# Kernel optimization log

Hardware: AMD Instinct MI355X
Metric: run time of the kernel (lower is better)

## Reference

```python
import jax, jax.numpy as jnp
import numpy as np

N = 100000        # nodes
E = 1600000       # edges (avg degree 16)
HID = 64          # hidden_dim
IN = 64           # input_dim
H = 4             # GAT heads
C = HID // H      # per-head channels (hidden//4)
LN_EPS = 1e-5
NEG_SLOPE = 0.2   # PyG GATConv default


def setup_inputs() -> dict:
    key = jax.random.key(0)
    ks = jax.random.split(key, 12)

    def nrm(k, shape, fan_in):
        return jax.random.normal(k, shape, jnp.float32) / np.sqrt(fan_in).astype(np.float32)

    x = jax.random.normal(ks[0], (N, IN), jnp.float32)
    edge_index = jax.random.randint(ks[1], (2, E), 0, N, jnp.int32)
    return {
        "x": x,
        "edge_index": edge_index,
        "emb_W": nrm(ks[2], (HID, IN), IN),
        "emb_b": jnp.zeros((HID,), jnp.float32),
        "e8_W": nrm(ks[3], (3, HID, HID), HID),
        "gat_W": nrm(ks[4], (3, HID, H * C), HID),
        "att_src": nrm(ks[5], (3, H, C), C),
        "att_dst": nrm(ks[6], (3, H, C), C),
        "gat_b": jnp.zeros((3, HID), jnp.float32),
        "fus_W": nrm(ks[7], (3, HID, 2 * HID), 2 * HID),
        "fus_b": jnp.zeros((3, HID), jnp.float32),
        "ln_g": jnp.ones((3, HID), jnp.float32),
        "ln_b": jnp.zeros((3, HID), jnp.float32),
        "r_W1": nrm(ks[8], (HID // 2, HID), HID),
        "r_b1": jnp.zeros((HID // 2,), jnp.float32),
        "r_W2": nrm(ks[9], (1, HID // 2), HID // 2),
        "r_b2": jnp.zeros((1,), jnp.float32),
    }


def _forward(x, edge_index, emb_W, emb_b, e8_W, gat_W, att_src, att_dst, gat_b,
             fus_W, fus_b, ln_g, ln_b, r_W1, r_b1, r_W2, r_b2):
    n = x.shape[0]
    row, col = edge_index[0], edge_index[1]

    # --- E8 symmetric normalization (depends only on graph; constant across layers) ---
    deg = jax.ops.segment_sum(jnp.ones_like(col, dtype=jnp.float32), col, num_segments=n)
    dinv = jnp.where(deg > 0, deg ** -0.5, 0.0)           # inf -> 0 as in torch code
    vals = dinv[row] * dinv[col]                           # [E]

    # --- GAT self-loops (PyG GATConv add_self_loops=True) ---
    loop = jnp.arange(n, dtype=row.dtype)
    src = jnp.concatenate([row, loop])                     # [E+N]
    dst = jnp.concatenate([col, loop])                     # [E+N]

    h = x @ emb_W.T + emb_b                                # embedding: [N, HID]

    for i in range(3):  # fixed 3 structurally-distinct blocks
        res = h
        # E8: sparse adj matmul then linear (no bias)
        x_e8 = jax.ops.segment_sum(vals[:, None] * h[col], row, num_segments=n) @ e8_W[i].T

        # GATConv (heads=4, concat)
        g = (h @ gat_W[i]).reshape(n, H, C)                # [N,H,C]
        a_s = (g * att_src[i]).sum(-1)                     # [N,H]
        a_d = (g * att_dst[i]).sum(-1)                     # [N,H]
        e = jax.nn.leaky_relu(a_s[src] + a_d[dst], NEG_SLOPE)   # [E+N,H]
        m = jax.lax.stop_gradient(jax.ops.segment_max(e, dst, num_segments=n))
        ee = jnp.exp(e - m[dst])
        s = jax.ops.segment_sum(ee, dst, num_segments=n)   # [N,H], >0 (self-loops)
        alpha = ee / s[dst]                                # per-dst softmax
        x_gat = jax.ops.segment_sum(alpha[:, :, None] * g[src], dst, num_segments=n)
        x_gat = x_gat.reshape(n, H * C) + gat_b[i]

        # fusion + residual + LayerNorm + ReLU (dropout is identity in eval)
        h = jnp.concatenate([x_e8, x_gat], axis=-1) @ fus_W[i].T + fus_b[i]
        h = h + res
        mu = h.mean(-1, keepdims=True)
        var = ((h - mu) ** 2).mean(-1, keepdims=True)
        h = (h - mu) * jax.lax.rsqrt(var + LN_EPS) * ln_g[i] + ln_b[i]
        h = jax.nn.relu(h)

    h1 = jax.nn.relu(h @ r_W1.T + r_b1)                    # [N, HID//2]
    return jax.nn.sigmoid(h1 @ r_W2.T + r_b2)              # [N, 1]


def reference(x, edge_index, emb_W, emb_b, e8_W, gat_W, att_src, att_dst, gat_b,
              fus_W, fus_b, ln_g, ln_b, r_W1, r_b1, r_W2, r_b2):
    return _forward(x, edge_index, emb_W, emb_b, e8_W, gat_W, att_src, att_dst, gat_b,
                    fus_W, fus_b, ln_g, ln_b, r_W1, r_b1, r_W2, r_b2)
```

## Files before the change

### kernel.cpp

```cpp
#include <hip/hip_runtime.h>
#include <hip/hip_bf16.h>
#include <hip/hip_fp16.h>

typedef __hip_bfloat16 bf16;
typedef unsigned short ushort_t;
typedef unsigned short us8 __attribute__((ext_vector_type(8)));
typedef _Float16 half8 __attribute__((ext_vector_type(8)));
typedef float f32x4 __attribute__((ext_vector_type(4)));

#define NEG 0.2f
#define LNEPS 1e-5f
#define BWD 512

__device__ __forceinline__ int plaus(unsigned int lo){
    lo &= 0x7FFFu;
    if (lo == 0) return 1;
    unsigned int ex = (lo >> 7) & 0xFF;
    return (ex >= 100 && ex <= 140) ? 1 : 0;
}

__device__ __forceinline__ float decode_slot(const ushort_t* s, long long i, int fl){
    long long base = i << fl;
    unsigned int hi = s[base + fl];
    unsigned int lo = s[base];
    unsigned int bits = (hi << 16) | (lo * (unsigned int)fl);
    return __uint_as_float(bits);
}

__device__ __forceinline__ unsigned encf(float f){
    int b = __float_as_int(f);
    return (b >= 0) ? ((unsigned)b | 0x80000000u) : (unsigned)(~b);
}
__device__ __forceinline__ float decf(unsigned k){
    return (k & 0x80000000u) ? __uint_as_float(k & 0x7FFFFFFFu)
                             : __uint_as_float(~k);
}

#define P_TOTAL 56577
#define CONV_BLKS 222
__global__ __launch_bounds__(256) void k_init(const void* p0, const void* p1, const void* p2,
        const void* p3, const void* p4, const void* p5, const void* p6, const void* p7,
        const void* p8, const void* p9, const void* p10, const void* p11, const void* p12,
        const void* p13, const void* p14, const void* xs,
        const int* __restrict__ row, const int* __restrict__ col, int E, int NBK,
        int* flags, float* P, int* bcnt, unsigned* mxsu){
    __shared__ int lh[512];
    int t = threadIdx.x;
    if (blockIdx.x >= CONV_BLKS){
        int hb = blockIdx.x - CONV_BLKS;
        for (int i = t; i < 2*NBK; i += 256) lh[i] = 0;
        __syncthreads();
        for (long long e = (long long)hb*256 + t; e < E; e += (long long)256*256){
            atomicAdd(&lh[row[e] >> 9], 1);
            atomicAdd(&lh[NBK + (col[e] >> 9)], 1);
        }
        __syncthreads();
        for (int i = t; i < 2*NBK; i += 256){
            int v = lh[i];
            if (v) atomicAdd(&bcnt[i], v);
        }
        return;
    }
    if (blockIdx.x == 0){
        if (t < 9){
            const void* dt[9] = {xs, p0, p2, p3, p4, p5, p7, p11, p13};
            const ushort_t* w = (const ushort_t*)dt[t];
            int all_bf = 1;
            for (int i = 0; i < 16; i++) all_bf &= plaus((unsigned int)w[i]);
            flags[t] = all_bf ? 0 : 1;
        } else if (t == 9){
            const ushort_t* w = (const ushort_t*)p9;
            flags[9] = (w[0] == 0x3F80u) ? 0 : 1;
        }
        if (t < 32) mxsu[t] = 0u;
    }
    int idx = blockIdx.x*256 + t;
    if (idx >= P_TOTAL) return;
    const int sizes[15] = {4096,64,12288,12288,192,192,192,24576,192,192,192,2048,32,32,1};
    const int fidx[15]  = {1,  -1,  2,    3,    4,  5,  -1, 6,    -1, 9,  -1, 7,   -1,8, -1};
    const void* ptrs[15] = {p0,p1,p2,p3,p4,p5,p6,p7,p8,p9,p10,p11,p12,p13,p14};
    int s = 0, base = 0;
    while (idx - base >= sizes[s]){ base += sizes[s]; s++; }
    int li = idx - base;
    int fi = fidx[s];
    int fl = 0;
    if (fi == 9){
        const ushort_t* w = (const ushort_t*)ptrs[s];
        fl = (w[0] == 0x3F80u) ? 0 : 1;
    } else if (fi >= 0){
        const ushort_t* w = (const ushort_t*)ptrs[s];
        int all_bf = 1;
        for (int i = 0; i < 16; i++) all_bf &= plaus((unsigned int)w[i]);
        fl = all_bf ? 0 : 1;
    }
    P[idx] = decode_slot((const ushort_t*)ptrs[s], li, fl);
}

#define PRW_B0 (3*8192)
#define PRW_B1 (PRW_B0 + 192)
#define PRW_B2 (PRW_B1 + 3*5120)
__global__ __launch_bounds__(256) void kb_scanprew(const int* __restrict__ bcnt,
        int* __restrict__ bptr_r, int* __restrict__ bptr_c,
        int* __restrict__ bcur_r, int* __restrict__ bcur_c, int NBK, int E,
        const float* __restrict__ fus_W, const float* __restrict__ e8_W,
        const float* __restrict__ gat_b, const float* __restrict__ fus_b,
        const float* __restrict__ gat_W, const float* __restrict__ att_src,
        const float* __restrict__ att_dst,
        _Float16* __restrict__ Bfrag, float* __restrict__ b2c, _Float16* __restrict__ Bg){
    __shared__ int sh[256];
    int t = threadIdx.x;
    if (blockIdx.x < 2){
        int side = blockIdx.x;
        const int* c = bcnt + side*NBK;
        int* bp = side ? bptr_c : bptr_r;
        int* bc = side ? bcur_c : bcur_r;
        int v = (t < NBK) ? c[t] : 0;
        sh[t] = v; __syncthreads();
        for (int off = 1; off < 256; off <<= 1){
            int add = (t >= off) ? sh[t-off] : 0;
            __syncthreads();
            sh[t] += add;
            __syncthreads();
        }
        if (t < NBK){ int e = sh[t] - v; bp[t] = e; bc[t] = e; }
        if (t == 0) bp[NBK] = E;
        return;
    }
    int idx = (blockIdx.x - 2)*256 + t;
    if (idx < PRW_B0){
        int i = idx / 8192; int rem = idx & 8191;
        int j = rem & 7, lane = (rem >> 3) & 63, kk = (rem >> 9) & 3, tt = rem >> 11;
        int k = kk*32 + (lane >> 4)*8 + j;
        int n = tt*16 + (lane & 15);
        float v;
        if (k < 64){
            const float* fw = fus_W + (size_t)i*8192 + (size_t)n*128;
            const float* ew = e8_W + (size_t)i*4096;
            float acc = 0.f;
            for (int p = 0; p < 64; p++) acc += fw[p] * ew[p*64 + k];
            v = acc;
        } else {
            v = fus_W[(size_t)i*8192 + (size_t)n*128 + 64 + (k - 64)];
        }
        Bfrag[idx] = (_Float16)v;
    } else if (idx < PRW_B1){
        int t2 = idx - PRW_B0;
        int i = t2 >> 6, j = t2 & 63;
        const float* fw = fus_W + (size_t)i*8192 + (size_t)j*128 + 64;
        float acc = fus_b[i*64+j];
        for (int p = 0; p < 64; p++) acc += gat_b[i*64+p] * fw[p];
        b2c[t2] = acc;
    } else if (idx < PRW_B2){
        int t3 = idx - PRW_B1;
        int i = t3 / 5120; int rem = t3 % 5120;
        int j = rem & 7, lane = (rem >> 3) & 63, kk = (rem >> 9) & 1, tt = rem >> 10;
        int k = kk*32 + (lane >> 4)*8 + j;
        int nn = lane & 15;
        float v;
        if (tt < 4){
            v = gat_W[(size_t)i*4096 + k*64 + (tt*16 + nn)];
        } else if (nn < 8){
            int hx = nn >> 1;
            const float* att = (nn & 1) ? att_dst : att_src;
            float acc = 0.f;
            for (int cc = 0; cc < 16; cc++)
                acc += gat_W[(size_t)i*4096 + k*64 + hx*16 + cc] * att[i*64 + hx*16 + cc];
            v = acc;
        } else {
            v = 0.f;
        }
        Bg[t3] = (_Float16)v;
    }
}

__global__ __launch_bounds__(1024) void kb_bin(const int* __restrict__ row,
        const int* __restrict__ col, int* __restrict__ bcur_r, int* __restrict__ bcur_c,
        uint2* __restrict__ stage_r, uint2* __restrict__ stage_c, int NBK, int E){
    __shared__ int lh[256], lbase[256];
    int side = blockIdx.x >> 8;
    int bid  = blockIdx.x & 255;
    const int* key = side ? col : row;
    const int* pay = side ? row : col;
    int* bcur = side ? bcur_c : bcur_r;
    uint2* stage = side ? stage_c : stage_r;
    int t = threadIdx.x;
    for (long long tile = (long long)bid*1024; tile < E; tile += (long long)256*1024){
        for (int i = t; i < NBK; i += 1024) lh[i] = 0;
        __syncthreads();
        int e = (int)tile + t;
        int k = 0, p = 0, b = -1, rank = 0;
        if (e < E){
            k = key[e]; p = pay[e]; b = k >> 9;
            rank = atomicAdd(&lh[b], 1);
        }
        __syncthreads();
        for (int i = t; i < NBK; i += 1024){
            int c = lh[i];
            lbase[i] = c ? atomicAdd(&bcur[i], c) : 0;
        }
        __syncthreads();
        if (b >= 0) stage[lbase[b] + rank] = make_uint2((unsigned)k, (unsigned)p);
        __syncthreads();
    }
}

__global__ __launch_bounds__(1024) void kb_place(const uint2* __restrict__ stage_r,
        const uint2* __restrict__ stage_c, const int* __restrict__ bptr_r,
        const int* __restrict__ bptr_c, int* __restrict__ ptr_r, int* __restrict__ ptr_c,
        int* __restrict__ re_col, int* __restrict__ ce_row,
        float* __restrict__ dinv, int NBK, int N, int E){
    __shared__ int lcnt[BWD], lsc[BWD], lcur[BWD];
    int side = blockIdx.x >= NBK;
    int b = blockIdx.x - (side ? NBK : 0);
    const uint2* stage = side ? stage_c : stage_r;
    const int* bptr = side ? bptr_c : bptr_r;
    int* ptr = side ? ptr_c : ptr_r;
    int* outarr = side ? ce_row : re_col;
    int wantdinv = side;
    int s = bptr[b], e = bptr[b+1];
    int nbase = b << 9;
    int t = threadIdx.x;
    if (t < BWD) lcnt[t] = 0;
    __syncthreads();
    for (int i = s + t; i < e; i += 1024)
        atomicAdd(&lcnt[stage[i].x - nbase], 1);
    __syncthreads();
    if (t < BWD) lsc[t] = lcnt[t];
    __syncthreads();
    for (int off = 1; off < BWD; off <<= 1){
        int add = (t >= off && t < BWD) ? lsc[t-off] : 0;
        __syncthreads();
        if (t < BWD) lsc[t] += add;
        __syncthreads();
    }
    if (t < BWD){
        int node = nbase + t;
        int excl = lsc[t] - lcnt[t];
        lcur[t] = excl;
        if (node < N){
            ptr[node] = s + excl;
            if (wantdinv) dinv[node] = lcnt[t] > 0 ? rsqrtf((float)lcnt[t]) : 0.f;
        }
    }
    if (b == 0 && t == 0) ptr[N] = E;
    __syncthreads();
    for (int i = s + t; i < e; i += 1024){
        uint2 rec = stage[i];
        int pos = s + atomicAdd(&lcur[rec.x - nbase], 1);
        outarr[pos] = (int)rec.y;
    }
}

__global__ __launch_bounds__(256) void k_embed_g(const ushort_t* __restrict__ xs,
        const int* __restrict__ flags, const float* __restrict__ W,
        const float* __restrict__ b, const float* __restrict__ dinv,
        const _Float16* __restrict__ Bgn,
        __half* __restrict__ h16, __half* __restrict__ ht16, __half* __restrict__ G16,
        float* __restrict__ a_s, float* __restrict__ a_d, float* __restrict__ mxs, int N){
    __shared__ float redm[4][8];
    __shared__ _Float16 tbuf[4][1024];
    int lane = threadIdx.x & 63;
    int wv = threadIdx.x >> 6;
    int q = lane >> 4, c = lane & 15;
    _Float16* tb = tbuf[wv];
    int fl = flags[0];
    half8 Be[4][2];
    #pragma unroll
    for (int t = 0; t < 4; t++){
        #pragma unroll
        for (int kk = 0; kk < 2; kk++){
            half8 v;
            #pragma unroll
            for (int j = 0; j < 8; j++)
                v[j] = (_Float16)W[(t*16 + c)*64 + kk*32 + q*8 + j];
            Be[t][kk] = v;
        }
    }
    half8 Bg[5][2];
    const half8* Bgp = (const half8*)Bgn;
    #pragma unroll
    for (int t = 0; t < 5; t++)
        #pragma unroll
        for (int kk = 0; kk < 2; kk++)
            Bg[t][kk] = Bgp[(t*2+kk)*64 + lane];
    float bj[4];
    #pragma unroll
    for (int t = 0; t < 4; t++) bj[t] = b[t*16 + c];
    float lmax = -1e30f;
    int tiles = (N + 15) >> 4;
    int wid = (blockIdx.x*blockDim.x + threadIdx.x) >> 6;
    int nw  = (gridDim.x*blockDim.x) >> 6;
    for (int tile = wid; tile < tiles; tile += nw){
        int nb = tile << 4;
        int anode = nb + c; if (anode >= N) anode = N - 1;
        half8 A0, A1;
        #pragma unroll
        for (int j = 0; j < 8; j++){
            A0[j] = (_Float16)decode_slot(xs, (long long)anode*64 + q*8 + j, fl);
            A1[j] = (_Float16)decode_slot(xs, (long long)anode*64 + 32 + q*8 + j, fl);
        }
        f32x4 acc[4];
        #pragma unroll
        for (int t = 0; t < 4; t++){
            f32x4 z = {0.f, 0.f, 0.f, 0.f};
            z = __builtin_amdgcn_mfma_f32_16x16x32_f16(A0, Be[t][0], z, 0, 0, 0);
            z = __builtin_amdgcn_mfma_f32_16x16x32_f16(A1, Be[t][1], z, 0, 0, 0);
            acc[t] = z;
        }
        #pragma unroll
        for (int r = 0; r < 4; r++){
            int node = nb + q*4 + r;
            int nd2 = q*4 + r;
            #pragma unroll
            for (int t = 0; t < 4; t++){
                float out = acc[t][r] + bj[t];
                int byte = nd2*128 + (t*16 + c)*2;
                byte ^= (nd2 & 7) << 4;
                *(_Float16*)((char*)tb + byte) = (_Float16)out;
                if (node < N){
                    h16[(size_t)node*64 + t*16 + c] = __float2half(out);
                    ht16[(size_t)node*64 + t*16 + c] = __float2half(dinv[node]*out);
                }
            }
        }
        int b0 = (c*128 + 16*q) ^ ((c & 7) << 4);
        int b1 = (c*128 + 64 + 16*q) ^ ((c & 7) << 4);
        half8 A0g = *(half8*)((char*)tb + b0);
        half8 A1g = *(half8*)((char*)tb + b1);
        f32x4 gacc[5];
        #pragma unroll
        for (int t = 0; t < 5; t++){
            f32x4 z = {0.f, 0.f, 0.f, 0.f};
            z = __builtin_amdgcn_mfma_f32_16x16x32_f16(A0g, Bg[t][0], z, 0, 0, 0);
            z = __builtin_amdgcn_mfma_f32_16x16x32_f16(A1g, Bg[t][1], z, 0, 0, 0);
            gacc[t] = z;
        }
        #pragma unroll
        for (int r = 0; r < 4; r++) lmax = fmaxf(lmax, gacc[4][r]);
        #pragma unroll
        for (int r = 0; r < 4; r++){
            int node = nb + q*4 + r;
            if (node < N){
                #pragma unroll
                for (int t = 0; t < 4; t++)
                    G16[(size_t)node*64 + t*16 + c] = __float2half(gacc[t][r]);
                if (c < 8){
                    int hx = c >> 1;
                    if (c & 1) a_d[node*4+hx] = gacc[4][r];
                    else       a_s[node*4+hx] = gacc[4][r];
                }
            }
        }
    }
    lmax = fmaxf(lmax, __shfl_xor(lmax, 16));
    lmax = fmaxf(lmax, __shfl_xor(lmax, 32));
    if (lane < 8) redm[wv][lane] = lmax;
    __syncthreads();
    if (threadIdx.x < 8){
        float m = fmaxf(fmaxf(redm[0][threadIdx.x], redm[1][threadIdx.x]),
                        fmaxf(redm[2][threadIdx.x], redm[3][threadIdx.x]));
        int hx = threadIdx.x >> 1;
        int ix = (threadIdx.x & 1) ? 4 + hx : hx;
        atomicMax((unsigned*)mxs + ix, encf(m));
    }
}

__device__ __forceinline__ float leaky(float t){ return t > 0.f ? t : NEG*t; }

__global__ __launch_bounds__(256) void k_gather(const __half* __restrict__ ht16,
        const __half* __restrict__ G16,
        const float* __restrict__ a_s, const float* __restrict__ a_d,
        const float* __restrict__ mxs, const float* __restrict__ dinv,
        const int* __restrict__ row_ptr, const int* __restrict__ re_col,
        const int* __restrict__ col_ptr, const int* __restrict__ ce_row,
        __half* __restrict__ Aj16, __half* __restrict__ xg16, int N){
    int lane = threadIdx.x & 63;
    int grp  = lane >> 3;
    int sub  = lane & 7;
    int hh   = sub >> 1;
    int wid  = (blockIdx.x*blockDim.x + threadIdx.x) >> 6;
    int v    = wid*8 + grp;
    if (v >= N) return;
    const us8* htb = (const us8*)ht16;
    const us8* gb  = (const us8*)G16;
    const unsigned* mu = (const unsigned*)mxs;
    float sh = leaky(decf(mu[hh]) + decf(mu[4+hh]));
    int rs = row_ptr[v], re = row_ptr[v+1];
    float a0[8] = {0,0,0,0,0,0,0,0}, a1[8] = {0,0,0,0,0,0,0,0};
    float a2[8] = {0,0,0,0,0,0,0,0}, a3[8] = {0,0,0,0,0,0,0,0};
    int i = rs;
    for (; i + 3 < re; i += 4){
        us8 q0 = htb[(size_t)re_col[i]*8 + sub];
        us8 q1 = htb[(size_t)re_col[i+1]*8 + sub];
        us8 q2 = htb[(size_t)re_col[i+2]*8 + sub];
        us8 q3 = htb[(size_t)re_col[i+3]*8 + sub];
        #pragma unroll
        for (int j = 0; j < 8; j++){
            a0[j] += __half2float(__ushort_as_half(q0[j]));
            a1[j] += __half2float(__ushort_as_half(q1[j]));
            a2[j] += __half2float(__ushort_as_half(q2[j]));
            a3[j] += __half2float(__ushort_as_half(q3[j]));
        }
    }
    for (; i < re; i++){
        us8 q0 = htb[(size_t)re_col[i]*8 + sub];
        #pragma unroll
        for (int j = 0; j < 8; j++) a0[j] += __half2float(__ushort_as_half(q0[j]));
    }
    float dv = dinv[v];
    us8 pa;
    #pragma unroll
    for (int j = 0; j < 8; j++)
        pa[j] = __half_as_ushort(__float2half(dv*((a0[j]+a1[j]) + (a2[j]+a3[j]))));
    ((us8*)Aj16)[(size_t)v*8 + sub] = pa;
    float adv = a_d[v*4+hh];
    float eesl = __expf(leaky(a_s[v*4+hh] + adv) - sh);
    float s0 = eesl, s1 = 0.f, s2 = 0.f, s3 = 0.f;
    {
        us8 g0 = gb[(size_t)v*8 + sub];
        #pragma unroll
        for (int j = 0; j < 8; j++){
            a0[j] = eesl * __half2float(__ushort_as_half(g0[j]));
            a1[j] = 0.f; a2[j] = 0.f; a3[j] = 0.f;
        }
    }
    int cs = col_ptr[v], ce = col_ptr[v+1];
    i = cs;
    for (; i + 3 < ce; i += 4){
        int r0 = ce_row[i], r1 = ce_row[i+1], r2 = ce_row[i+2], r3 = ce_row[i+3];
        float e0 = __expf(leaky(a_s[r0*4+hh] + adv) - sh);
        float e1 = __expf(leaky(a_s[r1*4+hh] + adv) - sh);
        float e2 = __expf(leaky(a_s[r2*4+hh] + adv) - sh);
        float e3 = __expf(leaky(a_s[r3*4+hh] + adv) - sh);
        us8 q0 = gb[(size_t)r0*8 + sub];
        us8 q1 = gb[(size_t)r1*8 + sub];
        us8 q2 = gb[(size_t)r2*8 + sub];
        us8 q3 = gb[(size_t)r3*8 + sub];
        #pragma unroll
        for (int j = 0; j < 8; j++){
            a0[j] += e0 * __half2float(__ushort_as_half(q0[j]));
            a1[j] += e1 * __half2float(__ushort_as_half(q1[j]));
            a2[j] += e2 * __half2float(__ushort_as_half(q2[j]));
            a3[j] += e3 * __half2float(__ushort_as_half(q3[j]));
        }
        s0 += e0; s1 += e1; s2 += e2; s3 += e3;
    }
    for (; i < ce; i++){
        int r0 = ce_row[i];
        float e0 = __expf(leaky(a_s[r0*4+hh] + adv) - sh);
        us8 q0 = gb[(size_t)r0*8 + sub];
        #pragma unroll
        for (int j = 0; j < 8; j++) a0[j] += e0 * __half2float(__ushort_as_half(q0[j]));
        s0 += e0;
    }
    float inv = 1.f/((s0+s1)+(s2+s3));
    us8 px;
    #pragma unroll
    for (int j = 0; j < 8; j++)
        px[j] = __half_as_ushort(__float2half(((a0[j]+a1[j]) + (a2[j]+a3[j]))*inv));
    ((us8*)xg16)[(size_t)v*8 + sub] = px;
}

__global__ __launch_bounds__(256) void k_fuse_g(
        const __half* __restrict__ Aj16, const __half* __restrict__ xg16,
        const float* __restrict__ dinv, __half* __restrict__ h16,
        __half* __restrict__ ht16,
        const _Float16* __restrict__ Bfrag, const float* __restrict__ b2c,
        const float* __restrict__ ln_g, const float* __restrict__ ln_b,
        const _Float16* __restrict__ Bgn, __half* __restrict__ G16,
        float* __restrict__ a_s, float* __restrict__ a_d,
        float* __restrict__ mxs_next, int N){
    __shared__ float redm[4][8];
    __shared__ _Float16 tbuf[4][1024];
    int lane = threadIdx.x & 63;
    int wv = threadIdx.x >> 6;
    int q = lane >> 4, c = lane & 15;
    _Float16* tb = tbuf[wv];
    half8 B[4][4];
    const half8* Bp = (const half8*)Bfrag;
    #pragma unroll
    for (int t = 0; t < 4; t++)
        #pragma unroll
        for (int kk = 0; kk < 4; kk++)
            B[t][kk] = Bp[(t*4+kk)*64 + lane];
    half8 Bg[5][2];
    const half8* Bgp = (const half8*)Bgn;
    #pragma unroll
    for (int t = 0; t < 5; t++)
        #pragma unroll
        for (int kk = 0; kk < 2; kk++)
            Bg[t][kk] = Bgp[(t*2+kk)*64 + lane];
    float bj[4], lg[4], lb[4];
    #pragma unroll
    for (int t = 0; t < 4; t++){
        int n = t*16 + c;
        bj[t] = b2c[n]; lg[t] = ln_g[n]; lb[t] = ln_b[n];
    }
    float lmax = -1e30f;
    int tiles = (N + 15) >> 4;
    int wid = (blockIdx.x*blockDim.x + threadIdx.x) >> 6;
    int nw  = (gridDim.x*blockDim.x) >> 6;
    for (int tile = wid; tile < tiles; tile += nw){
        int nb = tile << 4;
        int anode = nb + c; if (anode >= N) anode = N - 1;
        const half8* ap = (const half8*)(Aj16 + (size_t)anode*64);
        const half8* xp = (const half8*)(xg16 + (size_t)anode*64);
        half8 A0 = ap[q];
        half8 A1 = ap[4 + q];
        half8 A2 = xp[q];
        half8 A3 = xp[4 + q];
        f32x4 acc[4];
        #pragma unroll
        for (int t = 0; t < 4; t++){
            f32x4 z = {0.f, 0.f, 0.f, 0.f};
            z = __builtin_amdgcn_mfma_f32_16x16x32_f16(A0, B[t][0], z, 0, 0, 0);
            z = __builtin_amdgcn_mfma_f32_16x16x32_f16(A1, B[t][1], z, 0, 0, 0);
            z = __builtin_amdgcn_mfma_f32_16x16x32_f16(A2, B[t][2], z, 0, 0, 0);
            z = __builtin_amdgcn_mfma_f32_16x16x32_f16(A3, B[t][3], z, 0, 0, 0);
            acc[t] = z;
        }
        float y[4][4];
        #pragma unroll
        for (int r = 0; r < 4; r++){
            int node = nb + q*4 + r;
            int nd = node < N ? node : N - 1;
            #pragma unroll
            for (int t = 0; t < 4; t++)
                y[t][r] = acc[t][r] + bj[t]
                        + __half2float(h16[(size_t)nd*64 + t*16 + c]);
        }
        #pragma unroll
        for (int r = 0; r < 4; r++){
            int node = nb + q*4 + r;
            float s = (y[0][r] + y[1][r]) + (y[2][r] + y[3][r]);
            #pragma unroll
            for (int o = 1; o < 16; o <<= 1) s += __shfl_xor(s, o);
            float mu = s * (1.f/64.f);
            float d0 = y[0][r]-mu, d1 = y[1][r]-mu, d2 = y[2][r]-mu, d3 = y[3][r]-mu;
            float var = (d0*d0 + d1*d1) + (d2*d2 + d3*d3);
            #pragma unroll
            for (int o = 1; o < 16; o <<= 1) var += __shfl_xor(var, o);
            var *= (1.f/64.f);
            float rstd = rsqrtf(var + LNEPS);
            int nd2 = q*4 + r;
            #pragma unroll
            for (int t = 0; t < 4; t++){
                float out = (y[t][r]-mu)*rstd*lg[t] + lb[t];
                out = out > 0.f ? out : 0.f;
                int byte = nd2*128 + (t*16 + c)*2;
                byte ^= (nd2 & 7) << 4;
                *(_Float16*)((char*)tb + byte) = (_Float16)out;
                if (node < N){
                    h16[(size_t)node*64 + t*16 + c] = __float2half(out);
                    ht16[(size_t)node*64 + t*16 + c] = __float2half(dinv[node]*out);
                }
            }
        }
        int b0 = (c*128 + 16*q) ^ ((c & 7) << 4);
        int b1 = (c*128 + 64 + 16*q) ^ ((c & 7) << 4);
        half8 A0g = *(half8*)((char*)tb + b0);
        half8 A1g = *(half8*)((char*)tb + b1);
        f32x4 gacc[5];
        #pragma unroll
        for (int t = 0; t < 5; t++){
            f32x4 z = {0.f, 0.f, 0.f, 0.f};
            z = __builtin_amdgcn_mfma_f32_16x16x32_f16(A0g, Bg[t][0], z, 0, 0, 0);
            z = __builtin_amdgcn_mfma_f32_16x16x32_f16(A1g, Bg[t][1], z, 0, 0, 0);
            gacc[t] = z;
        }
        #pragma unroll
        for (int r = 0; r < 4; r++) lmax = fmaxf(lmax, gacc[4][r]);
        #pragma unroll
        for (int r = 0; r < 4; r++){
            int node = nb + q*4 + r;
            if (node < N){
                #pragma unroll
                for (int t = 0; t < 4; t++)
                    G16[(size_t)node*64 + t*16 + c] = __float2half(gacc[t][r]);
                if (c < 8){
                    int hx = c >> 1;
                    if (c & 1) a_d[node*4+hx] = gacc[4][r];
                    else       a_s[node*4+hx] = gacc[4][r];
                }
            }
        }
    }
    lmax = fmaxf(lmax, __shfl_xor(lmax, 16));
    lmax = fmaxf(lmax, __shfl_xor(lmax, 32));
    if (lane < 8) redm[wv][lane] = lmax;
    __syncthreads();
    if (threadIdx.x < 8){
        float m = fmaxf(fmaxf(redm[0][threadIdx.x], redm[1][threadIdx.x]),
                        fmaxf(redm[2][threadIdx.x], redm[3][threadIdx.x]));
        int hx = threadIdx.x >> 1;
        int ix = (threadIdx.x & 1) ? 4 + hx : hx;
        atomicMax((unsigned*)mxs_next + ix, encf(m));
    }
}

__global__ __launch_bounds__(256) void k_fuse_ro(
        const __half* __restrict__ Aj16, const __half* __restrict__ xg16,
        const __half* __restrict__ h16,
        const _Float16* __restrict__ Bfrag, const float* __restrict__ b2c,
        const float* __restrict__ ln_g, const float* __restrict__ ln_b,
        const float* __restrict__ rW1, const float* __restrict__ rb1,
        const float* __restrict__ rW2, const float* __restrict__ rb2,
        float* __restrict__ out, int N){
    __shared__ _Float16 tbuf[4][1024];
    int lane = threadIdx.x & 63;
    int wv = threadIdx.x >> 6;
    int q = lane >> 4, c = lane & 15;
    _Float16* tb = tbuf[wv];
    half8 B[4][4];
    const half8* Bp = (const half8*)Bfrag;
    #pragma unroll
    for (int t = 0; t < 4; t++)
        #pragma unroll
        for (int kk = 0; kk < 4; kk++)
            B[t][kk] = Bp[(t*4+kk)*64 + lane];
    half8 B1r[2][2];
    #pragma unroll
    for (int t = 0; t < 2; t++){
        #pragma unroll
        for (int kk = 0; kk < 2; kk++){
            half8 v;
            #pragma unroll
            for (int j = 0; j < 8; j++)
                v[j] = (_Float16)rW1[(t*16 + c)*64 + kk*32 + q*8 + j];
            B1r[t][kk] = v;
        }
    }
    float bj[4], lg[4], lb[4];
    #pragma unroll
    for (int t = 0; t < 4; t++){
        int n = t*16 + c;
        bj[t] = b2c[n]; lg[t] = ln_g[n]; lb[t] = ln_b[n];
    }
    float b1v[2] = {rb1[c], rb1[16 + c]};
    float w2a = rW2[c], w2b = rW2[16 + c];
    float b2v = rb2[0];
    int tiles = (N + 15) >> 4;
    int wid = (blockIdx.x*blockDim.x + threadIdx.x) >> 6;
    int nw  = (gridDim.x*blockDim.x) >> 6;
    for (int tile = wid; tile < tiles; tile += nw){
        int nb = tile << 4;
        int anode = nb + c; if (anode >= N) anode = N - 1;
        const half8* ap = (const half8*)(Aj16 + (size_t)anode*64);
        const half8* xp = (const half8*)(xg16 + (size_t)anode*64);
        half8 A0 = ap[q];
        half8 A1 = ap[4 + q];
        half8 A2 = xp[q];
        half8 A3 = xp[4 + q];
        f32x4 acc[4];
        #pragma unroll
        for (int t = 0; t < 4; t++){
            f32x4 z = {0.f, 0.f, 0.f, 0.f};
            z = __builtin_amdgcn_mfma_f32_16x16x32_f16(A0, B[t][0], z, 0, 0, 0);
            z = __builtin_amdgcn_mfma_f32_16x16x32_f16(A1, B[t][1], z, 0, 0, 0);
            z = __builtin_amdgcn_mfma_f32_16x16x32_f16(A2, B[t][2], z, 0, 0, 0);
            z = __builtin_amdgcn_mfma_f32_16x16x32_f16(A3, B[t][3], z, 0, 0, 0);
            acc[t] = z;
        }
        float y[4][4];
        #pragma unroll
        for (int r = 0; r < 4; r++){
            int node = nb + q*4 + r;
            int nd = node < N ? node : N - 1;
            #pragma unroll
            for (int t = 0; t < 4; t++)
                y[t][r] = acc[t][r] + bj[t]
                        + __half2float(h16[(size_t)nd*64 + t*16 + c]);
        }
        #pragma unroll
        for (int r = 0; r < 4; r++){
            float s = (y[0][r] + y[1][r]) + (y[2][r] + y[3][r]);
            #pragma unroll
            for (int o = 1; o < 16; o <<= 1) s += __shfl_xor(s, o);
            float mu = s * (1.f/64.f);
            float d0 = y[0][r]-mu, d1 = y[1][r]-mu, d2 = y[2][r]-mu, d3 = y[3][r]-mu;
            float var = (d0*d0 + d1*d1) + (d2*d2 + d3*d3);
            #pragma unroll
            for (int o = 1; o < 16; o <<= 1) var += __shfl_xor(var, o);
            var *= (1.f/64.f);
            float rstd = rsqrtf(var + LNEPS);
            int nd2 = q*4 + r;
            #pragma unroll
            for (int t = 0; t < 4; t++){
                float outv = (y[t][r]-mu)*rstd*lg[t] + lb[t];
                outv = outv > 0.f ? outv : 0.f;
                int byte = nd2*128 + (t*16 + c)*2;
                byte ^= (nd2 & 7) << 4;
                *(_Float16*)((char*)tb + byte) = (_Float16)outv;
            }
        }
        int b0 = (c*128 + 16*q) ^ ((c & 7) << 4);
        int b1 = (c*128 + 64 + 16*q) ^ ((c & 7) << 4);
        half8 A0g = *(half8*)((char*)tb + b0);
        half8 A1g = *(half8*)((char*)tb + b1);
        f32x4 racc[2];
        #pragma unroll
        for (int t = 0; t < 2; t++){
            f32x4 z = {0.f, 0.f, 0.f, 0.f};
            z = __builtin_amdgcn_mfma_f32_16x16x32_f16(A0g, B1r[t][0], z, 0, 0, 0);
            z = __builtin_amdgcn_mfma_f32_16x16x32_f16(A1g, B1r[t][1], z, 0, 0, 0);
            racc[t] = z;
        }
        #pragma unroll
        for (int r = 0; r < 4; r++){
            int node = nb + q*4 + r;
            float h1a = racc[0][r] + b1v[0]; h1a = h1a > 0.f ? h1a : 0.f;
            float h1b = racc[1][r] + b1v[1]; h1b = h1b > 0.f ? h1b : 0.f;
            float p = h1a*w2a + h1b*w2b;
            p += __shfl_xor(p, 1);
            p += __shfl_xor(p, 2);
            p += __shfl_xor(p, 4);
            p += __shfl_xor(p, 8);
            if (c == 0 && node < N){
                float z = p + b2v;
                out[node] = 1.f/(1.f + __expf(-z));
            }
        }
    }
}

extern "C" void kernel_launch(void* const* d_in, const int* in_sizes, int n_in,
                              void* d_out, int out_size, void* d_ws, size_t ws_size,
                              hipStream_t stream){
    const ushort_t* xs = (const ushort_t*)d_in[0];
    const int*      ei = (const int*)d_in[1];

    int N = in_sizes[0] / 64;
    int E = in_sizes[1] / 2;
    const int* row = ei;
    const int* col = ei + E;
    int NBK = (N + BWD - 1) / BWD;

    size_t stageF = (size_t)2*E;
    size_t mirF   = (size_t)N*32;
    size_t aliasF = stageF > mirF ? stageF : mirF;

    float* f = (float*)d_ws;
    size_t o = 0;
    int*   flags = (int*)(f + o); o += 16;
    float* P     = f + o; o += P_TOTAL + 63;
    __half* h16  = (__half*)(f + o); o += mirF;
    __half* ht16 = (__half*)(f + o); o += mirF;
    __half* G16  = (__half*)(f + o); o += mirF;
    __half* Aj16 = (__half*)(f + o); size_t aoff = o; o += aliasF;
    __half* xg16 = (__half*)(f + o); size_t xoff = o; o += aliasF;
    uint2* stage_r = (uint2*)(f + aoff);
    uint2* stage_c = (uint2*)(f + xoff);
    float* a_s   = f + o; o += (size_t)N*4;
    float* a_d   = f + o; o += (size_t)N*4;
    float* mxs   = f + o; o += 32;
    float* dinv  = f + o; o += ((size_t)N + 15) & ~15ull;
    int* bcnt    = (int*)(f + o); o += 512;
    int* bptr_r  = (int*)(f + o); o += 512;
    int* bptr_c  = (int*)(f + o); o += 512;
    int* bcur_r  = (int*)(f + o); o += 512;
    int* bcur_c  = (int*)(f + o); o += 512;
    int* ptr_r   = (int*)(f + o); o += ((size_t)N + 16) & ~15ull;
    int* ptr_c   = (int*)(f + o); o += ((size_t)N + 16) & ~15ull;
    int* re_col  = (int*)(f + o); o += (size_t)E;
    int* ce_row  = (int*)(f + o); o += (size_t)E;
    float* b2c   = f + o; o += 3*64;
    _Float16* Bfrag = (_Float16*)(f + o); o += 3*4096;
    _Float16* Bg    = (_Float16*)(f + o); o += 3*2560;

    const float* emb_W   = P + 0;
    const float* emb_b   = P + 4096;
    const float* e8_W    = P + 4160;
    const float* gat_W   = P + 16448;
    const float* att_src = P + 28736;
    const float* att_dst = P + 28928;
    const float* gat_b   = P + 29120;
    const float* fus_W   = P + 29312;
    const float* fus_b   = P + 53888;
    const float* ln_g    = P + 54080;
    const float* ln_b    = P + 54272;
    const float* r_W1    = P + 54464;
    const float* r_b1    = P + 56512;
    const float* r_W2    = P + 56544;
    const float* r_b2    = P + 56576;

    hipMemsetAsync(bcnt, 0, 512*sizeof(int), stream);
    k_init<<<CONV_BLKS + 256, 256, 0, stream>>>(
        d_in[2],d_in[3],d_in[4],d_in[5],d_in[6],d_in[7],d_in[8],d_in[9],
        d_in[10],d_in[11],d_in[12],d_in[13],d_in[14],d_in[15],d_in[16],
        d_in[0], row, col, E, NBK, flags, P, bcnt, (unsigned*)mxs);

    int prwblk = (PRW_B2 + 255) / 256;
    kb_scanprew<<<2 + prwblk, 256, 0, stream>>>(bcnt, bptr_r, bptr_c, bcur_r, bcur_c,
                                                NBK, E, fus_W, e8_W, gat_b, fus_b,
                                                gat_W, att_src, att_dst, Bfrag, b2c, Bg);
    kb_bin<<<512, 1024, 0, stream>>>(row, col, bcur_r, bcur_c, stage_r, stage_c, NBK, E);
    kb_place<<<2*NBK, 1024, 0, stream>>>(stage_r, stage_c, bptr_r, bptr_c,
                                         ptr_r, ptr_c, re_col, ce_row, dinv, NBK, N, E);

    int tiles = (N + 15) / 16;
    int fgrid = (tiles + 7) / 8;
    int ggrid = (N + 31) / 32;
    k_embed_g<<<fgrid, 256, 0, stream>>>(xs, flags, emb_W, emb_b, dinv, Bg,
                                         h16, ht16, G16, a_s, a_d, mxs, N);
    for (int i = 0; i < 3; i++){
        k_gather<<<ggrid, 256, 0, stream>>>(ht16, G16, a_s, a_d, mxs + i*8, dinv,
                                            ptr_r, re_col, ptr_c, ce_row,
                                            Aj16, xg16, N);
        if (i < 2){
            k_fuse_g<<<fgrid, 256, 0, stream>>>(Aj16, xg16, dinv, h16, ht16,
                                                Bfrag + (size_t)i*8192, b2c + i*64,
                                                ln_g + i*64, ln_b + i*64,
                                                Bg + (size_t)(i+1)*5120, G16,
                                                a_s, a_d, mxs + (i+1)*8, N);
        } else {
            k_fuse_ro<<<fgrid, 256, 0, stream>>>(Aj16, xg16, h16,
                                                 Bfrag + (size_t)i*8192, b2c + i*64,
                                                 ln_g + i*64, ln_b + i*64,
                                                 r_W1, r_b1, r_W2, r_b2,
                                                 (float*)d_out, N);
        }
    }
}
```

Before: 651.6 us.

## Fuse gather with fusion/LayerNorm epilogue and split GAT projection kernel

The per-node gather of E8 and GAT aggregates is merged with the fusion matmul, residual, LayerNorm and ReLU, and the readout, using scalar FMAs over weights held in LDS. This removes the Aj16/xg16 intermediate round-trips through global memory. The next layer's GAT projection moves into a separate MFMA kernel, k_gat_g, and h/ht are ping-ponged between two buffers. The change also packs staging records into 32 bits and vectorises input loads in the embedding, at the cost of replacing MFMA with per-lane scalar FMA for the 128x64 fusion matmul and adding an LDS-heavy inner loop.

```diff
diff --git a/kernel.cpp b/kernel.cpp
--- a/kernel.cpp
+++ b/kernel.cpp
@@ -6,6 +6,7 @@
 typedef unsigned short ushort_t;
 typedef unsigned short us8 __attribute__((ext_vector_type(8)));
 typedef _Float16 half8 __attribute__((ext_vector_type(8)));
+typedef _Float16 half4v __attribute__((ext_vector_type(4)));
 typedef float f32x4 __attribute__((ext_vector_type(4)));
 
 #define NEG 0.2f
@@ -99,14 +100,16 @@
 #define PRW_B0 (3*8192)
 #define PRW_B1 (PRW_B0 + 192)
 #define PRW_B2 (PRW_B1 + 3*5120)
+#define PRW_B3 (PRW_B2 + 2048)
 __global__ __launch_bounds__(256) void kb_scanprew(const int* __restrict__ bcnt,
         int* __restrict__ bptr_r, int* __restrict__ bptr_c,
         int* __restrict__ bcur_r, int* __restrict__ bcur_c, int NBK, int E,
         const float* __restrict__ fus_W, const float* __restrict__ e8_W,
         const float* __restrict__ gat_b, const float* __restrict__ fus_b,
         const float* __restrict__ gat_W, const float* __restrict__ att_src,
-        const float* __restrict__ att_dst,
-        _Float16* __restrict__ Bfrag, float* __restrict__ b2c, _Float16* __restrict__ Bg){
+        const float* __restrict__ att_dst, const float* __restrict__ r_W1,
+        _Float16* __restrict__ Wt16, float* __restrict__ b2c,
+        _Float16* __restrict__ Bg, _Float16* __restrict__ Wr16){
     __shared__ int sh[256];
     int t = threadIdx.x;
     if (blockIdx.x < 2){
@@ -129,20 +132,18 @@
     int idx = (blockIdx.x - 2)*256 + t;
     if (idx < PRW_B0){
         int i = idx / 8192; int rem = idx & 8191;
-        int j = rem & 7, lane = (rem >> 3) & 63, kk = (rem >> 9) & 3, tt = rem >> 11;
-        int k = kk*32 + (lane >> 4)*8 + j;
-        int n = tt*16 + (lane & 15);
+        int p = rem >> 6, j = rem & 63;
         float v;
-        if (k < 64){
-            const float* fw = fus_W + (size_t)i*8192 + (size_t)n*128;
+        if (p < 64){
+            const float* fw = fus_W + (size_t)i*8192 + (size_t)j*128;
             const float* ew = e8_W + (size_t)i*4096;
             float acc = 0.f;
-            for (int p = 0; p < 64; p++) acc += fw[p] * ew[p*64 + k];
+            for (int q = 0; q < 64; q++) acc += fw[q] * ew[q*64 + p];
             v = acc;
         } else {
-            v = fus_W[(size_t)i*8192 + (size_t)n*128 + 64 + (k - 64)];
-        }
-        Bfrag[idx] = (_Float16)v;
+            v = fus_W[(size_t)i*8192 + (size_t)j*128 + p];
+        }
+        Wt16[idx] = (_Float16)v;
     } else if (idx < PRW_B1){
         int t2 = idx - PRW_B0;
         int i = t2 >> 6, j = t2 & 63;
@@ -170,19 +171,23 @@
             v = 0.f;
         }
         Bg[t3] = (_Float16)v;
+    } else if (idx < PRW_B3){
+        int t4 = idx - PRW_B2;
+        int k = t4 >> 5, j = t4 & 31;
+        Wr16[t4] = (_Float16)r_W1[j*64 + k];
     }
 }
 
 __global__ __launch_bounds__(1024) void kb_bin(const int* __restrict__ row,
         const int* __restrict__ col, int* __restrict__ bcur_r, int* __restrict__ bcur_c,
-        uint2* __restrict__ stage_r, uint2* __restrict__ stage_c, int NBK, int E){
+        unsigned* __restrict__ stage_r, unsigned* __restrict__ stage_c, int NBK, int E){
     __shared__ int lh[256], lbase[256];
     int side = blockIdx.x >> 8;
     int bid  = blockIdx.x & 255;
     const int* key = side ? col : row;
     const int* pay = side ? row : col;
     int* bcur = side ? bcur_c : bcur_r;
-    uint2* stage = side ? stage_c : stage_r;
+    unsigned* stage = side ? stage_c : stage_r;
     int t = threadIdx.x;
     for (long long tile = (long long)bid*1024; tile < E; tile += (long long)256*1024){
         for (int i = t; i < NBK; i += 1024) lh[i] = 0;
@@ -199,31 +204,30 @@
             lbase[i] = c ? atomicAdd(&bcur[i], c) : 0;
         }
         __syncthreads();
-        if (b >= 0) stage[lbase[b] + rank] = make_uint2((unsigned)k, (unsigned)p);
+        if (b >= 0) stage[lbase[b] + rank] = ((unsigned)(k & 511) << 23) | (unsigned)p;
         __syncthreads();
     }
 }
 
-__global__ __launch_bounds__(1024) void kb_place(const uint2* __restrict__ stage_r,
-        const uint2* __restrict__ stage_c, const int* __restrict__ bptr_r,
+__global__ __launch_bounds__(1024) void kb_place(const unsigned* __restrict__ stage_r,
+        const unsigned* __restrict__ stage_c, const int* __restrict__ bptr_r,
         const int* __restrict__ bptr_c, int* __restrict__ ptr_r, int* __restrict__ ptr_c,
         int* __restrict__ re_col, int* __restrict__ ce_row,
         float* __restrict__ dinv, int NBK, int N, int E){
     __shared__ int lcnt[BWD], lsc[BWD], lcur[BWD];
     int side = blockIdx.x >= NBK;
     int b = blockIdx.x - (side ? NBK : 0);
-    const uint2* stage = side ? stage_c : stage_r;
+    const unsigned* stage = side ? stage_c : stage_r;
     const int* bptr = side ? bptr_c : bptr_r;
     int* ptr = side ? ptr_c : ptr_r;
     int* outarr = side ? ce_row : re_col;
     int wantdinv = side;
     int s = bptr[b], e = bptr[b+1];
-    int nbase = b << 9;
     int t = threadIdx.x;
     if (t < BWD) lcnt[t] = 0;
     __syncthreads();
     for (int i = s + t; i < e; i += 1024)
-        atomicAdd(&lcnt[stage[i].x - nbase], 1);
+        atomicAdd(&lcnt[stage[i] >> 23], 1);
     __syncthreads();
     if (t < BWD) lsc[t] = lcnt[t];
     __syncthreads();
@@ -234,7 +238,7 @@
         __syncthreads();
     }
     if (t < BWD){
-        int node = nbase + t;
+        int node = (b << 9) + t;
         int excl = lsc[t] - lcnt[t];
         lcur[t] = excl;
         if (node < N){
@@ -245,9 +249,9 @@
     if (b == 0 && t == 0) ptr[N] = E;
     __syncthreads();
     for (int i = s + t; i < e; i += 1024){
-        uint2 rec = stage[i];
-        int pos = s + atomicAdd(&lcur[rec.x - nbase], 1);
-        outarr[pos] = (int)rec.y;
+        unsigned rec = stage[i];
+        int pos = s + atomicAdd(&lcur[rec >> 23], 1);
+        outarr[pos] = (int)(rec & 0x7FFFFFu);
     }
 }
 
@@ -294,10 +298,26 @@
         int nb = tile << 4;
         int anode = nb + c; if (anode >= N) anode = N - 1;
         half8 A0, A1;
-        #pragma unroll
-        for (int j = 0; j < 8; j++){
-            A0[j] = (_Float16)decode_slot(xs, (long long)anode*64 + q*8 + j, fl);
-            A1[j] = (_Float16)decode_slot(xs, (long long)anode*64 + 32 + q*8 + j, fl);
+        if (fl == 0){
+            const us8* xv = (const us8*)xs;
+            us8 r0 = xv[(size_t)anode*8 + q];
+            us8 r1 = xv[(size_t)anode*8 + 4 + q];
+            #pragma unroll
+            for (int j = 0; j < 8; j++){
+                A0[j] = (_Float16)__uint_as_float((unsigned)r0[j] << 16);
+                A1[j] = (_Float16)__uint_as_float((unsigned)r1[j] << 16);
+            }
+        } else {
+            const f32x4* xf = (const f32x4*)xs;
+            f32x4 f0 = xf[(size_t)anode*16 + q*2];
+            f32x4 f1 = xf[(size_t)anode*16 + q*2 + 1];
+            f32x4 f2 = xf[(size_t)anode*16 + 8 + q*2];
+            f32x4 f3 = xf[(size_t)anode*16 + 8 + q*2 + 1];
+            #pragma unroll
+            for (int j = 0; j < 4; j++){
+                A0[j] = (_Float16)f0[j]; A0[4+j] = (_Float16)f1[j];
+                A1[j] = (_Float16)f2[j]; A1[4+j] = (_Float16)f3[j];
+            }
         }
         f32x4 acc[4];
         #pragma unroll
@@ -365,26 +385,98 @@
     }
 }
 
+__global__ __launch_bounds__(256) void k_gat_g(const __half* __restrict__ h16,
+        const _Float16* __restrict__ Bg, __half* __restrict__ G16,
+        float* __restrict__ a_s, float* __restrict__ a_d, float* __restrict__ mxs, int N){
+    __shared__ float redm[4][8];
+    int lane = threadIdx.x & 63;
+    int wv = threadIdx.x >> 6;
+    int q = lane >> 4, c = lane & 15;
+    half8 B[5][2];
+    const half8* Bp = (const half8*)Bg;
+    #pragma unroll
+    for (int t = 0; t < 5; t++)
+        #pragma unroll
+        for (int kk = 0; kk < 2; kk++)
+            B[t][kk] = Bp[(t*2+kk)*64 + lane];
+    float lmax = -1e30f;
+    int tiles = (N + 15) >> 4;
+    int wid = (blockIdx.x*blockDim.x + threadIdx.x) >> 6;
+    int nw  = (gridDim.x*blockDim.x) >> 6;
+    for (int tile = wid; tile < tiles; tile += nw){
+        int nb = tile << 4;
+        int anode = nb + c; if (anode >= N) anode = N - 1;
+        const half8* ap = (const half8*)(h16 + (size_t)anode*64);
+        half8 A0 = ap[q];
+        half8 A1 = ap[4 + q];
+        f32x4 acc[5];
+        #pragma unroll
+        for (int t = 0; t < 5; t++){
+            f32x4 z = {0.f, 0.f, 0.f, 0.f};
+            z = __builtin_amdgcn_mfma_f32_16x16x32_f16(A0, B[t][0], z, 0, 0, 0);
+            z = __builtin_amdgcn_mfma_f32_16x16x32_f16(A1, B[t][1], z, 0, 0, 0);
+            acc[t] = z;
+        }
+        #pragma unroll
+        for (int r = 0; r < 4; r++) lmax = fmaxf(lmax, acc[4][r]);
+        #pragma unroll
+        for (int r = 0; r < 4; r++){
+            int node = nb + q*4 + r;
+            if (node < N){
+                #pragma unroll
+                for (int t = 0; t < 4; t++)
+                    G16[(size_t)node*64 + t*16 + c] = __float2half(acc[t][r]);
+                if (c < 8){
+                    int hx = c >> 1;
+                    if (c & 1) a_d[node*4+hx] = acc[4][r];
+                    else       a_s[node*4+hx] = acc[4][r];
+                }
+            }
+        }
+    }
+    lmax = fmaxf(lmax, __shfl_xor(lmax, 16));
+    lmax = fmaxf(lmax, __shfl_xor(lmax, 32));
+    if (lane < 8) redm[wv][lane] = lmax;
+    __syncthreads();
+    if (threadIdx.x < 8){
+        float m = fmaxf(fmaxf(redm[0][threadIdx.x], redm[1][threadIdx.x]),
+                        fmaxf(redm[2][threadIdx.x], redm[3][threadIdx.x]));
+        int hx = threadIdx.x >> 1;
+        int ix = (threadIdx.x & 1) ? 4 + hx : hx;
+        atomicMax((unsigned*)mxs + ix, encf(m));
+    }
+}
+
 __device__ __forceinline__ float leaky(float t){ return t > 0.f ? t : NEG*t; }
 
-__global__ __launch_bounds__(256) void k_gather(const __half* __restrict__ ht16,
+__global__ __launch_bounds__(256) void k_gfuse(
+        const __half* __restrict__ ht_src, const __half* __restrict__ h_src,
         const __half* __restrict__ G16,
         const float* __restrict__ a_s, const float* __restrict__ a_d,
         const float* __restrict__ mxs, const float* __restrict__ dinv,
         const int* __restrict__ row_ptr, const int* __restrict__ re_col,
         const int* __restrict__ col_ptr, const int* __restrict__ ce_row,
-        __half* __restrict__ Aj16, __half* __restrict__ xg16, int N){
+        const _Float16* __restrict__ Wt16, const float* __restrict__ b2c,
+        const float* __restrict__ ln_g, const float* __restrict__ ln_b,
+        __half* __restrict__ h_dst, __half* __restrict__ ht_dst, int N){
+    __shared__ _Float16 Wl[8192];
+    __shared__ _Float16 inb[4][8][128];
+    {
+        const half8* src = (const half8*)Wt16;
+        half8* dst = (half8*)Wl;
+        for (int i = threadIdx.x; i < 1024; i += 256) dst[i] = src[i];
+    }
+    __syncthreads();
     int lane = threadIdx.x & 63;
-    int grp  = lane >> 3;
-    int sub  = lane & 7;
-    int hh   = sub >> 1;
-    int wid  = (blockIdx.x*blockDim.x + threadIdx.x) >> 6;
-    int v    = wid*8 + grp;
+    int wv = threadIdx.x >> 6;
+    int grp = lane >> 3, sub = lane & 7, hh = sub >> 1;
+    int wid = (blockIdx.x*blockDim.x + threadIdx.x) >> 6;
+    int v = wid*8 + grp;
     if (v >= N) return;
-    const us8* htb = (const us8*)ht16;
+    const us8* htb = (const us8*)ht_src;
     const us8* gb  = (const us8*)G16;
-    const unsigned* mu = (const unsigned*)mxs;
-    float sh = leaky(decf(mu[hh]) + decf(mu[4+hh]));
+    const unsigned* mup = (const unsigned*)mxs;
+    float sh = leaky(decf(mup[hh]) + decf(mup[4+hh]));
     int rs = row_ptr[v], re = row_ptr[v+1];
     float a0[8] = {0,0,0,0,0,0,0,0}, a1[8] = {0,0,0,0,0,0,0,0};
     float a2[8] = {0,0,0,0,0,0,0,0}, a3[8] = {0,0,0,0,0,0,0,0};
@@ -408,11 +500,9 @@
         for (int j = 0; j < 8; j++) a0[j] += __half2float(__ushort_as_half(q0[j]));
     }
     float dv = dinv[v];
-    us8 pa;
-    #pragma unroll
-    for (int j = 0; j < 8; j++)
-        pa[j] = __half_as_ushort(__float2half(dv*((a0[j]+a1[j]) + (a2[j]+a3[j]))));
-    ((us8*)Aj16)[(size_t)v*8 + sub] = pa;
+    float ajv[8];
+    #pragma unroll
+    for (int j = 0; j < 8; j++) ajv[j] = dv*((a0[j]+a1[j]) + (a2[j]+a3[j]));
     float adv = a_d[v*4+hh];
     float eesl = __expf(leaky(a_s[v*4+hh] + adv) - sh);
     float s0 = eesl, s1 = 0.f, s2 = 0.f, s3 = 0.f;
@@ -454,273 +544,215 @@
         s0 += e0;
     }
     float inv = 1.f/((s0+s1)+(s2+s3));
-    us8 px;
+    _Float16* myin = inb[wv][grp];
+    half8 ha, hx;
+    #pragma unroll
+    for (int j = 0; j < 8; j++){
+        ha[j] = (_Float16)ajv[j];
+        hx[j] = (_Float16)(((a0[j]+a1[j]) + (a2[j]+a3[j]))*inv);
+    }
+    *(half8*)(myin + sub*8)      = ha;
+    *(half8*)(myin + 64 + sub*8) = hx;
+    float y[8];
+    us8 hr = ((const us8*)h_src)[(size_t)v*8 + sub];
     #pragma unroll
     for (int j = 0; j < 8; j++)
-        px[j] = __half_as_ushort(__float2half(((a0[j]+a1[j]) + (a2[j]+a3[j]))*inv));
-    ((us8*)xg16)[(size_t)v*8 + sub] = px;
-}
-
-__global__ __launch_bounds__(256) void k_fuse_g(
-        const __half* __restrict__ Aj16, const __half* __restrict__ xg16,
-        const float* __restrict__ dinv, __half* __restrict__ h16,
-        __half* __restrict__ ht16,
-        const _Float16* __restrict__ Bfrag, const float* __restrict__ b2c,
+        y[j] = b2c[sub*8+j] + __half2float(__ushort_as_half(hr[j]));
+    for (int pp = 0; pp < 16; pp++){
+        half8 ib = *(half8*)(myin + pp*8);
+        #pragma unroll
+        for (int e = 0; e < 8; e++){
+            float xin = (float)ib[e];
+            half8 w = *(half8*)(Wl + (pp*8+e)*64 + sub*8);
+            #pragma unroll
+            for (int j = 0; j < 8; j++) y[j] += xin * (float)w[j];
+        }
+    }
+    float s = ((y[0]+y[1])+(y[2]+y[3])) + ((y[4]+y[5])+(y[6]+y[7]));
+    s += __shfl_xor(s, 1); s += __shfl_xor(s, 2); s += __shfl_xor(s, 4);
+    float mu = s * (1.f/64.f);
+    float var = 0.f;
+    #pragma unroll
+    for (int j = 0; j < 8; j++){ float d = y[j]-mu; var += d*d; }
+    var += __shfl_xor(var, 1); var += __shfl_xor(var, 2); var += __shfl_xor(var, 4);
+    var *= (1.f/64.f);
+    float rstd = rsqrtf(var + LNEPS);
+    us8 ho, hto;
+    #pragma unroll
+    for (int j = 0; j < 8; j++){
+        float o = (y[j]-mu)*rstd*ln_g[sub*8+j] + ln_b[sub*8+j];
+        o = o > 0.f ? o : 0.f;
+        ho[j]  = __half_as_ushort(__float2half(o));
+        hto[j] = __half_as_ushort(__float2half(dv*o));
+    }
+    ((us8*)h_dst)[(size_t)v*8 + sub]  = ho;
+    ((us8*)ht_dst)[(size_t)v*8 + sub] = hto;
+}
+
+__global__ __launch_bounds__(256) void k_gfuse_ro(
+        const __half* __restrict__ ht_src, const __half* __restrict__ h_src,
+        const __half* __restrict__ G16,
+        const float* __restrict__ a_s, const float* __restrict__ a_d,
+        const float* __restrict__ mxs, const float* __restrict__ dinv,
+        const int* __restrict__ row_ptr, const int* __restrict__ re_col,
+        const int* __restrict__ col_ptr, const int* __restrict__ ce_row,
+        const _Float16* __restrict__ Wt16, const float* __restrict__ b2c,
         const float* __restrict__ ln_g, const float* __restrict__ ln_b,
-        const _Float16* __restrict__ Bgn, __half* __restrict__ G16,
-        float* __restrict__ a_s, float* __restrict__ a_d,
-        float* __restrict__ mxs_next, int N){
-    __shared__ float redm[4][8];
-    __shared__ _Float16 tbuf[4][1024];
+        const _Float16* __restrict__ Wr16, const float* __restrict__ rb1,
+        const float* __restrict__ rW2, const float* __restrict__ rb2,
+        float* __restrict__ out, int N){
+    __shared__ _Float16 Wl[8192];
+    __shared__ _Float16 Wr[2048];
+    __shared__ _Float16 inb[4][8][128];
+    {
+        const half8* src = (const half8*)Wt16;
+        half8* dst = (half8*)Wl;
+        for (int i = threadIdx.x; i < 1024; i += 256) dst[i] = src[i];
+        const half8* src2 = (const half8*)Wr16;
+        half8* dst2 = (half8*)Wr;
+        for (int i = threadIdx.x; i < 256; i += 256) dst2[i] = src2[i];
+    }
+    __syncthreads();
     int lane = threadIdx.x & 63;
     int wv = threadIdx.x >> 6;
-    int q = lane >> 4, c = lane & 15;
-    _Float16* tb = tbuf[wv];
-    half8 B[4][4];
-    const half8* Bp = (const half8*)Bfrag;
-    #pragma unroll
-    for (int t = 0; t < 4; t++)
-        #pragma unroll
-        for (int kk = 0; kk < 4; kk++)
-            B[t][kk] = Bp[(t*4+kk)*64 + lane];
-    half8 Bg[5][2];
-    const half8* Bgp = (const half8*)Bgn;
-    #pragma unroll
-    for (int t = 0; t < 5; t++)
-        #pragma unroll
-        for (int kk = 0; kk < 2; kk++)
-            Bg[t][kk] = Bgp[(t*2+kk)*64 + lane];
-    float bj[4], lg[4], lb[4];
-    #pragma unroll
-    for (int t = 0; t < 4; t++){
-        int n = t*16 + c;
-        bj[t] = b2c[n]; lg[t] = ln_g[n]; lb[t] = ln_b[n];
-    }
-    float lmax = -1e30f;
-    int tiles = (N + 15) >> 4;
+    int grp = lane >> 3, sub = lane & 7, hh = sub >> 1;
     int wid = (blockIdx.x*blockDim.x + threadIdx.x) >> 6;
-    int nw  = (gridDim.x*blockDim.x) >> 6;
-    for (int tile = wid; tile < tiles; tile += nw){
-        int nb = tile << 4;
-        int anode = nb + c; if (anode >= N) anode = N - 1;
-        const half8* ap = (const half8*)(Aj16 + (size_t)anode*64);
-        const half8* xp = (const half8*)(xg16 + (size_t)anode*64);
-        half8 A0 = ap[q];
-        half8 A1 = ap[4 + q];
-        half8 A2 = xp[q];
-        half8 A3 = xp[4 + q];
-        f32x4 acc[4];
-        #pragma unroll
-        for (int t = 0; t < 4; t++){
-            f32x4 z = {0.f, 0.f, 0.f, 0.f};
-            z = __builtin_amdgcn_mfma_f32_16x16x32_f16(A0, B[t][0], z, 0, 0, 0);
-            z = __builtin_amdgcn_mfma_f32_16x16x32_f16(A1, B[t][1], z, 0, 0, 0);
-            z = __builtin_amdgcn_mfma_f32_16x16x32_f16(A2, B[t][2], z, 0, 0, 0);
-            z = __builtin_amdgcn_mfma_f32_16x16x32_f16(A3, B[t][3], z, 0, 0, 0);
-            acc[t] = z;
-        }
-        float y[4][4];
-        #pragma unroll
-        for (int r = 0; r < 4; r++){
-            int node = nb + q*4 + r;
-            int nd = node < N ? node : N - 1;
+    int v = wid*8 + grp;
+    if (v >= N) return;
+    const us8* htb = (const us8*)ht_src;
+    const us8* gb  = (const us8*)G16;
+    const unsigned* mup = (const unsigned*)mxs;
+    float sh = leaky(decf(mup[hh]) + decf(mup[4+hh]));
+    int rs = row_ptr[v], re = row_ptr[v+1];
+    float a0[8] = {0,0,0,0,0,0,0,0}, a1[8] = {0,0,0,0,0,0,0,0};
+    float a2[8] = {0,0,0,0,0,0,0,0}, a3[8] = {0,0,0,0,0,0,0,0};
+    int i = rs;
+    for (; i + 3 < re; i += 4){
+        us8 q0 = htb[(size_t)re_col[i]*8 + sub];
+        us8 q1 = htb[(size_t)re_col[i+1]*8 + sub];
+        us8 q2 = htb[(size_t)re_col[i+2]*8 + sub];
+        us8 q3 = htb[(size_t)re_col[i+3]*8 + sub];
+        #pragma unroll
+        for (int j = 0; j < 8; j++){
+            a0[j] += __half2float(__ushort_as_half(q0[j]));
+            a1[j] += __half2float(__ushort_as_half(q1[j]));
+            a2[j] += __half2float(__ushort_as_half(q2[j]));
+            a3[j] += __half2float(__ushort_as_half(q3[j]));
+        }
+    }
+    for (; i < re; i++){
+        us8 q0 = htb[(size_t)re_col[i]*8 + sub];
+        #pragma unroll
+        for (int j = 0; j < 8; j++) a0[j] += __half2float(__ushort_as_half(q0[j]));
+    }
+    float dv = dinv[v];
+    float ajv[8];
+    #pragma unroll
+    for (int j = 0; j < 8; j++) ajv[j] = dv*((a0[j]+a1[j]) + (a2[j]+a3[j]));
+    float adv = a_d[v*4+hh];
+    float eesl = __expf(leaky(a_s[v*4+hh] + adv) - sh);
+    float s0 = eesl, s1 = 0.f, s2 = 0.f, s3 = 0.f;
+    {
+        us8 g0 = gb[(size_t)v*8 + sub];
+        #pragma unroll
+        for (int j = 0; j < 8; j++){
+            a0[j] = eesl * __half2float(__ushort_as_half(g0[j]));
+            a1[j] = 0.f; a2[j] = 0.f; a3[j] = 0.f;
+        }
+    }
+    int cs = col_ptr[v], ce = col_ptr[v+1];
+    i = cs;
+    for (; i + 3 < ce; i += 4){
+        int r0 = ce_row[i], r1 = ce_row[i+1], r2 = ce_row[i+2], r3 = ce_row[i+3];
+        float e0 = __expf(leaky(a_s[r0*4+hh] + adv) - sh);
+        float e1 = __expf(leaky(a_s[r1*4+hh] + adv) - sh);
+        float e2 = __expf(leaky(a_s[r2*4+hh] + adv) - sh);
+        float e3 = __expf(leaky(a_s[r3*4+hh] + adv) - sh);
+        us8 q0 = gb[(size_t)r0*8 + sub];
+        us8 q1 = gb[(size_t)r1*8 + sub];
+        us8 q2 = gb[(size_t)r2*8 + sub];
+        us8 q3 = gb[(size_t)r3*8 + sub];
+        #pragma unroll
+        for (int j = 0; j < 8; j++){
+            a0[j] += e0 * __half2float(__ushort_as_half(q0[j]));
+            a1[j] += e1 * __half2float(__ushort_as_half(q1[j]));
+            a2[j] += e2 * __half2float(__ushort_as_half(q2[j]));
+            a3[j] += e3 * __half2float(__ushort_as_half(q3[j]));
+        }
+        s0 += e0; s1 += e1; s2 += e2; s3 += e3;
+    }
+    for (; i < ce; i++){
+        int r0 = ce_row[i];
+        float e0 = __expf(leaky(a_s[r0*4+hh] + adv) - sh);
+        us8 q0 = gb[(size_t)r0*8 + sub];
+        #pragma unroll
+        for (int j = 0; j < 8; j++) a0[j] += e0 * __half2float(__ushort_as_half(q0[j]));
+        s0 += e0;
+    }
+    float inv = 1.f/((s0+s1)+(s2+s3));
+    _Float16* myin = inb[wv][grp];
+    half8 ha, hx;
+    #pragma unroll
+    for (int j = 0; j < 8; j++){
+        ha[j] = (_Float16)ajv[j];
+        hx[j] = (_Float16)(((a0[j]+a1[j]) + (a2[j]+a3[j]))*inv);
+    }
+    *(half8*)(myin + sub*8)      = ha;
+    *(half8*)(myin + 64 + sub*8) = hx;
+    float y[8];
+    us8 hr = ((const us8*)h_src)[(size_t)v*8 + sub];
+    #pragma unroll
+    for (int j = 0; j < 8; j++)
+        y[j] = b2c[sub*8+j] + __half2float(__ushort_as_half(hr[j]));
+    for (int pp = 0; pp < 16; pp++){
+        half8 ib = *(half8*)(myin + pp*8);
+        #pragma unroll
+        for (int e = 0; e < 8; e++){
+            float xin = (float)ib[e];
+            half8 w = *(half8*)(Wl + (pp*8+e)*64 + sub*8);
             #pragma unroll
-            for (int t = 0; t < 4; t++)
-                y[t][r] = acc[t][r] + bj[t]
-                        + __half2float(h16[(size_t)nd*64 + t*16 + c]);
-        }
-        #pragma unroll
-        for (int r = 0; r < 4; r++){
-            int node = nb + q*4 + r;
-            float s = (y[0][r] + y[1][r]) + (y[2][r] + y[3][r]);
+            for (int j = 0; j < 8; j++) y[j] += xin * (float)w[j];
+        }
+    }
+    float s = ((y[0]+y[1])+(y[2]+y[3])) + ((y[4]+y[5])+(y[6]+y[7]));
+    s += __shfl_xor(s, 1); s += __shfl_xor(s, 2); s += __shfl_xor(s, 4);
+    float mu = s * (1.f/64.f);
+    float var = 0.f;
+    #pragma unroll
+    for (int j = 0; j < 8; j++){ float d = y[j]-mu; var += d*d; }
+    var += __shfl_xor(var, 1); var += __shfl_xor(var, 2); var += __shfl_xor(var, 4);
+    var *= (1.f/64.f);
+    float rstd = rsqrtf(var + LNEPS);
+    half8 hov;
+    #pragma unroll
+    for (int j = 0; j < 8; j++){
+        float o = (y[j]-mu)*rstd*ln_g[sub*8+j] + ln_b[sub*8+j];
+        o = o > 0.f ? o : 0.f;
+        hov[j] = (_Float16)o;
+    }
+    *(half8*)(myin + sub*8) = hov;
+    float h1[4];
+    #pragma unroll
+    for (int m = 0; m < 4; m++) h1[m] = rb1[sub*4+m];
+    for (int pp = 0; pp < 8; pp++){
+        half8 ib = *(half8*)(myin + pp*8);
+        #pragma unroll
+        for (int e = 0; e < 8; e++){
+            float xin = (float)ib[e];
+            half4v wr = *(half4v*)(Wr + (pp*8+e)*32 + sub*4);
             #pragma unroll
-            for (int o = 1; o < 16; o <<= 1) s += __shfl_xor(s, o);
-            float mu = s * (1.f/64.f);
-            float d0 = y[0][r]-mu, d1 = y[1][r]-mu, d2 = y[2][r]-mu, d3 = y[3][r]-mu;
-            float var = (d0*d0 + d1*d1) + (d2*d2 + d3*d3);
-            #pragma unroll
-            for (int o = 1; o < 16; o <<= 1) var += __shfl_xor(var, o);
-            var *= (1.f/64.f);
-            float rstd = rsqrtf(var + LNEPS);
-            int nd2 = q*4 + r;
-            #pragma unroll
-            for (int t = 0; t < 4; t++){
-                float out = (y[t][r]-mu)*rstd*lg[t] + lb[t];
-                out = out > 0.f ? out : 0.f;
-                int byte = nd2*128 + (t*16 + c)*2;
-                byte ^= (nd2 & 7) << 4;
-                *(_Float16*)((char*)tb + byte) = (_Float16)out;
-                if (node < N){
-                    h16[(size_t)node*64 + t*16 + c] = __float2half(out);
-                    ht16[(size_t)node*64 + t*16 + c] = __float2half(dinv[node]*out);
-                }
-            }
-        }
-        int b0 = (c*128 + 16*q) ^ ((c & 7) << 4);
-        int b1 = (c*128 + 64 + 16*q) ^ ((c & 7) << 4);
-        half8 A0g = *(half8*)((char*)tb + b0);
-        half8 A1g = *(half8*)((char*)tb + b1);
-        f32x4 gacc[5];
-        #pragma unroll
-        for (int t = 0; t < 5; t++){
-            f32x4 z = {0.f, 0.f, 0.f, 0.f};
-            z = __builtin_amdgcn_mfma_f32_16x16x32_f16(A0g, Bg[t][0], z, 0, 0, 0);
-            z = __builtin_amdgcn_mfma_f32_16x16x32_f16(A1g, Bg[t][1], z, 0, 0, 0);
-            gacc[t] = z;
-        }
-        #pragma unroll
-        for (int r = 0; r < 4; r++) lmax = fmaxf(lmax, gacc[4][r]);
-        #pragma unroll
-        for (int r = 0; r < 4; r++){
-            int node = nb + q*4 + r;
-            if (node < N){
-                #pragma unroll
-                for (int t = 0; t < 4; t++)
-                    G16[(size_t)node*64 + t*16 + c] = __float2half(gacc[t][r]);
-                if (c < 8){
-                    int hx = c >> 1;
-                    if (c & 1) a_d[node*4+hx] = gacc[4][r];
-                    else       a_s[node*4+hx] = gacc[4][r];
-                }
-            }
-        }
-    }
-    lmax = fmaxf(lmax, __shfl_xor(lmax, 16));
-    lmax = fmaxf(lmax, __shfl_xor(lmax, 32));
-    if (lane < 8) redm[wv][lane] = lmax;
-    __syncthreads();
-    if (threadIdx.x < 8){
-        float m = fmaxf(fmaxf(redm[0][threadIdx.x], redm[1][threadIdx.x]),
-                        fmaxf(redm[2][threadIdx.x], redm[3][threadIdx.x]));
-        int hx = threadIdx.x >> 1;
-        int ix = (threadIdx.x & 1) ? 4 + hx : hx;
-        atomicMax((unsigned*)mxs_next + ix, encf(m));
-    }
-}
-
-__global__ __launch_bounds__(256) void k_fuse_ro(
-        const __half* __restrict__ Aj16, const __half* __restrict__ xg16,
-        const __half* __restrict__ h16,
-        const _Float16* __restrict__ Bfrag, const float* __restrict__ b2c,
-        const float* __restrict__ ln_g, const float* __restrict__ ln_b,
-        const float* __restrict__ rW1, const float* __restrict__ rb1,
-        const float* __restrict__ rW2, const float* __restrict__ rb2,
-        float* __restrict__ out, int N){
-    __shared__ _Float16 tbuf[4][1024];
-    int lane = threadIdx.x & 63;
-    int wv = threadIdx.x >> 6;
-    int q = lane >> 4, c = lane & 15;
-    _Float16* tb = tbuf[wv];
-    half8 B[4][4];
-    const half8* Bp = (const half8*)Bfrag;
-    #pragma unroll
-    for (int t = 0; t < 4; t++)
-        #pragma unroll
-        for (int kk = 0; kk < 4; kk++)
-            B[t][kk] = Bp[(t*4+kk)*64 + lane];
-    half8 B1r[2][2];
-    #pragma unroll
-    for (int t = 0; t < 2; t++){
-        #pragma unroll
-        for (int kk = 0; kk < 2; kk++){
-            half8 v;
-            #pragma unroll
-            for (int j = 0; j < 8; j++)
-                v[j] = (_Float16)rW1[(t*16 + c)*64 + kk*32 + q*8 + j];
-            B1r[t][kk] = v;
-        }
-    }
-    float bj[4], lg[4], lb[4];
-    #pragma unroll
-    for (int t = 0; t < 4; t++){
-        int n = t*16 + c;
-        bj[t] = b2c[n]; lg[t] = ln_g[n]; lb[t] = ln_b[n];
-    }
-    float b1v[2] = {rb1[c], rb1[16 + c]};
-    float w2a = rW2[c], w2b = rW2[16 + c];
-    float b2v = rb2[0];
-    int tiles = (N + 15) >> 4;
-    int wid = (blockIdx.x*blockDim.x + threadIdx.x) >> 6;
-    int nw  = (gridDim.x*blockDim.x) >> 6;
-    for (int tile = wid; tile < tiles; tile += nw){
-        int nb = tile << 4;
-        int anode = nb + c; if (anode >= N) anode = N - 1;
-        const half8* ap = (const half8*)(Aj16 + (size_t)anode*64);
-        const half8* xp = (const half8*)(xg16 + (size_t)anode*64);
-        half8 A0 = ap[q];
-        half8 A1 = ap[4 + q];
-        half8 A2 = xp[q];
-        half8 A3 = xp[4 + q];
-        f32x4 acc[4];
-        #pragma unroll
-        for (int t = 0; t < 4; t++){
-            f32x4 z = {0.f, 0.f, 0.f, 0.f};
-            z = __builtin_amdgcn_mfma_f32_16x16x32_f16(A0, B[t][0], z, 0, 0, 0);
-            z = __builtin_amdgcn_mfma_f32_16x16x32_f16(A1, B[t][1], z, 0, 0, 0);
-            z = __builtin_amdgcn_mfma_f32_16x16x32_f16(A2, B[t][2], z, 0, 0, 0);
-            z = __builtin_amdgcn_mfma_f32_16x16x32_f16(A3, B[t][3], z, 0, 0, 0);
-            acc[t] = z;
-        }
-        float y[4][4];
-        #pragma unroll
-        for (int r = 0; r < 4; r++){
-            int node = nb + q*4 + r;
-            int nd = node < N ? node : N - 1;
-            #pragma unroll
-            for (int t = 0; t < 4; t++)
-                y[t][r] = acc[t][r] + bj[t]
-                        + __half2float(h16[(size_t)nd*64 + t*16 + c]);
-        }
-        #pragma unroll
-        for (int r = 0; r < 4; r++){
-            float s = (y[0][r] + y[1][r]) + (y[2][r] + y[3][r]);
-            #pragma unroll
-            for (int o = 1; o < 16; o <<= 1) s += __shfl_xor(s, o);
-            float mu = s * (1.f/64.f);
-            float d0 = y[0][r]-mu, d1 = y[1][r]-mu, d2 = y[2][r]-mu, d3 = y[3][r]-mu;
-            float var = (d0*d0 + d1*d1) + (d2*d2 + d3*d3);
-            #pragma unroll
-            for (int o = 1; o < 16; o <<= 1) var += __shfl_xor(var, o);
-            var *= (1.f/64.f);
-            float rstd = rsqrtf(var + LNEPS);
-            int nd2 = q*4 + r;
-            #pragma unroll
-            for (int t = 0; t < 4; t++){
-                float outv = (y[t][r]-mu)*rstd*lg[t] + lb[t];
-                outv = outv > 0.f ? outv : 0.f;
-                int byte = nd2*128 + (t*16 + c)*2;
-                byte ^= (nd2 & 7) << 4;
-                *(_Float16*)((char*)tb + byte) = (_Float16)outv;
-            }
-        }
-        int b0 = (c*128 + 16*q) ^ ((c & 7) << 4);
-        int b1 = (c*128 + 64 + 16*q) ^ ((c & 7) << 4);
-        half8 A0g = *(half8*)((char*)tb + b0);
-        half8 A1g = *(half8*)((char*)tb + b1);
-        f32x4 racc[2];
-        #pragma unroll
-        for (int t = 0; t < 2; t++){
-            f32x4 z = {0.f, 0.f, 0.f, 0.f};
-            z = __builtin_amdgcn_mfma_f32_16x16x32_f16(A0g, B1r[t][0], z, 0, 0, 0);
-            z = __builtin_amdgcn_mfma_f32_16x16x32_f16(A1g, B1r[t][1], z, 0, 0, 0);
-            racc[t] = z;
-        }
-        #pragma unroll
-        for (int r = 0; r < 4; r++){
-            int node = nb + q*4 + r;
-            float h1a = racc[0][r] + b1v[0]; h1a = h1a > 0.f ? h1a : 0.f;
-            float h1b = racc[1][r] + b1v[1]; h1b = h1b > 0.f ? h1b : 0.f;
-            float p = h1a*w2a + h1b*w2b;
-            p += __shfl_xor(p, 1);
-            p += __shfl_xor(p, 2);
-            p += __shfl_xor(p, 4);
-            p += __shfl_xor(p, 8);
-            if (c == 0 && node < N){
-                float z = p + b2v;
-                out[node] = 1.f/(1.f + __expf(-z));
-            }
-        }
-    }
+            for (int m = 0; m < 4; m++) h1[m] += xin * (float)wr[m];
+        }
+    }
+    float p = 0.f;
+    #pragma unroll
+    for (int m = 0; m < 4; m++){
+        float t = h1[m] > 0.f ? h1[m] : 0.f;
+        p += t * rW2[sub*4+m];
+    }
+    p += __shfl_xor(p, 1); p += __shfl_xor(p, 2); p += __shfl_xor(p, 4);
+    if (sub == 0)
+        out[v] = 1.f/(1.f + __expf(-(p + rb2[0])));
 }
 
 extern "C" void kernel_launch(void* const* d_in, const int* in_sizes, int n_in,
@@ -735,21 +767,19 @@
     const int* col = ei + E;
     int NBK = (N + BWD - 1) / BWD;
 
-    size_t stageF = (size_t)2*E;
-    size_t mirF   = (size_t)N*32;
-    size_t aliasF = stageF > mirF ? stageF : mirF;
+    size_t mirF = (size_t)N*32;
 
     float* f = (float*)d_ws;
     size_t o = 0;
     int*   flags = (int*)(f + o); o += 16;
     float* P     = f + o; o += P_TOTAL + 63;
-    __half* h16  = (__half*)(f + o); o += mirF;
-    __half* ht16 = (__half*)(f + o); o += mirF;
+    __half* h16a  = (__half*)(f + o); o += mirF;
+    __half* ht16a = (__half*)(f + o); o += mirF;
+    __half* h16b  = (__half*)(f + o); size_t boff = o; o += mirF;
+    __half* ht16b = (__half*)(f + o); size_t coff = o; o += mirF;
+    unsigned* stage_r = (unsigned*)(f + boff);
+    unsigned* stage_c = (unsigned*)(f + coff);
     __half* G16  = (__half*)(f + o); o += mirF;
-    __half* Aj16 = (__half*)(f + o); size_t aoff = o; o += aliasF;
-    __half* xg16 = (__half*)(f + o); size_t xoff = o; o += aliasF;
-    uint2* stage_r = (uint2*)(f + aoff);
-    uint2* stage_c = (uint2*)(f + xoff);
     float* a_s   = f + o; o += (size_t)N*4;
     float* a_d   = f + o; o += (size_t)N*4;
     float* mxs   = f + o; o += 32;
@@ -764,8 +794,9 @@
     int* re_col  = (int*)(f + o); o += (size_t)E;
     int* ce_row  = (int*)(f + o); o += (size_t)E;
     float* b2c   = f + o; o += 3*64;
-    _Float16* Bfrag = (_Float16*)(f + o); o += 3*4096;
-    _Float16* Bg    = (_Float16*)(f + o); o += 3*2560;
+    _Float16* Wt16 = (_Float16*)(f + o); o += 3*4096;
+    _Float16* Bg   = (_Float16*)(f + o); o += 3*2560;
+    _Float16* Wr16 = (_Float16*)(f + o); o += 1024;
 
     const float* emb_W   = P + 0;
     const float* emb_b   = P + 4096;
@@ -789,10 +820,11 @@
         d_in[10],d_in[11],d_in[12],d_in[13],d_in[14],d_in[15],d_in[16],
         d_in[0], row, col, E, NBK, flags, P, bcnt, (unsigned*)mxs);
 
-    int prwblk = (PRW_B2 + 255) / 256;
+    int prwblk = (PRW_B3 + 255) / 256;
     kb_scanprew<<<2 + prwblk, 256, 0, stream>>>(bcnt, bptr_r, bptr_c, bcur_r, bcur_c,
                                                 NBK, E, fus_W, e8_W, gat_b, fus_b,
-                                                gat_W, att_src, att_dst, Bfrag, b2c, Bg);
+                                                gat_W, att_src, att_dst, r_W1,
+                                                Wt16, b2c, Bg, Wr16);
     kb_bin<<<512, 1024, 0, stream>>>(row, col, bcur_r, bcur_c, stage_r, stage_c, NBK, E);
     kb_place<<<2*NBK, 1024, 0, stream>>>(stage_r, stage_c, bptr_r, bptr_c,
                                          ptr_r, ptr_c, re_col, ce_row, dinv, NBK, N, E);
@@ -801,23 +833,18 @@
     int fgrid = (tiles + 7) / 8;
     int ggrid = (N + 31) / 32;
     k_embed_g<<<fgrid, 256, 0, stream>>>(xs, flags, emb_W, emb_b, dinv, Bg,
-                                         h16, ht16, G16, a_s, a_d, mxs, N);
-    for (int i = 0; i < 3; i++){
-        k_gather<<<ggrid, 256, 0, stream>>>(ht16, G16, a_s, a_d, mxs + i*8, dinv,
-                                            ptr_r, re_col, ptr_c, ce_row,
-                                            Aj16, xg16, N);
-        if (i < 2){
-            k_fuse_g<<<fgrid, 256, 0, stream>>>(Aj16, xg16, dinv, h16, ht16,
-                                                Bfrag + (size_t)i*8192, b2c + i*64,
-                                                ln_g + i*64, ln_b + i*64,
-                                                Bg + (size_t)(i+1)*5120, G16,
-                                                a_s, a_d, mxs + (i+1)*8, N);
-        } else {
-            k_fuse_ro<<<fgrid, 256, 0, stream>>>(Aj16, xg16, h16,
-                                                 Bfrag + (size_t)i*8192, b2c + i*64,
-                                                 ln_g + i*64, ln_b + i*64,
-                                                 r_W1, r_b1, r_W2, r_b2,
-                                                 (float*)d_out, N);
-        }
-    }
-}
+                                         h16a, ht16a, G16, a_s, a_d, mxs, N);
+    k_gfuse<<<ggrid, 256, 0, stream>>>(ht16a, h16a, G16, a_s, a_d, mxs, dinv,
+                                       ptr_r, re_col, ptr_c, ce_row,
+                                       Wt16, b2c, ln_g, ln_b, h16b, ht16b, N);
+    k_gat_g<<<fgrid, 256, 0, stream>>>(h16b, Bg + 5120, G16, a_s, a_d, mxs + 8, N);
+    k_gfuse<<<ggrid, 256, 0, stream>>>(ht16b, h16b, G16, a_s, a_d, mxs + 8, dinv,
+                                       ptr_r, re_col, ptr_c, ce_row,
+                                       Wt16 + 8192, b2c + 64, ln_g + 64, ln_b + 64,
+                                       h16a, ht16a, N);
+    k_gat_g<<<fgrid, 256, 0, stream>>>(h16a, Bg + 2*5120, G16, a_s, a_d, mxs + 16, N);
+    k_gfuse_ro<<<ggrid, 256, 0, stream>>>(ht16a, h16a, G16, a_s, a_d, mxs + 16, dinv,
+                                          ptr_r, re_col, ptr_c, ce_row,
+                                          Wt16 + 2*8192, b2c + 128, ln_g + 128, ln_b + 128,
+                                          Wr16, r_b1, r_W2, r_b2, (float*)d_out, N);
+}
```

Measured after the change: 669.8 us. 2.8% more time.
